# Kernel tuning notes

Measured on AMD Instinct MI355X. Metric: run time of the kernel, lower is better.

## Reference

```python
import jax, jax.numpy as jnp
import numpy as np

N_NODES = 50000
N_EDGES = 800000
D_IN = 128
D_OUT = 128


def setup_inputs() -> dict:
    key = jax.random.key(0)
    k1, k2, k3, k4, k5 = jax.random.split(key, 5)
    gain = float(np.sqrt(2.0))  # calculate_gain('relu')
    # xavier_uniform bound: gain * sqrt(6/(fan_in+fan_out))
    bound = gain * float(np.sqrt(6.0 / (D_IN + D_OUT)))
    feat = jax.random.normal(k1, (N_NODES, D_IN), dtype=jnp.float32)
    weight = jax.random.uniform(k2, (D_IN, D_OUT), minval=-bound, maxval=bound, dtype=jnp.float32)
    loop_weight = jax.random.uniform(k3, (D_IN, D_OUT), minval=-bound, maxval=bound, dtype=jnp.float32)
    h_bias = jnp.zeros((D_OUT,), dtype=jnp.float32)
    src = jax.random.randint(k4, (N_EDGES,), 0, N_NODES, dtype=jnp.int32)
    dst = jax.random.randint(k5, (N_EDGES,), 0, N_NODES, dtype=jnp.int32)
    return {"feat": feat, "weight": weight, "h_bias": h_bias,
            "loop_weight": loop_weight, "src": src, "dst": dst}


def reference(feat, weight, h_bias, loop_weight, src, dst):
    # message: m_e = feat[src_e] @ W ; aggregate: h_v = sum_{e: dst_e=v} m_e
    # (equivalently transform-then-gather, which avoids the [E, D] matmul)
    transformed = feat @ weight                    # [N, D_out]
    msgs = transformed[src]                        # [E, D_out] gather
    h = jax.ops.segment_sum(msgs, dst, num_segments=feat.shape[0])  # [N, D_out]
    h = h + h_bias                                 # bias
    h = h + feat @ loop_weight                     # self-loop
    # activation=None, dropout=0 -> identity
    return h
```

## Files before the change

### kernel.cpp

```cpp
#include <hip/hip_runtime.h>

#define D 128
#define CAP 64
#define FCHUNK 4096
#define LROW 264

typedef __attribute__((ext_vector_type(8))) short bf16x8;
typedef __attribute__((ext_vector_type(4))) float f32x4;

__device__ inline unsigned short f2bf_rne(float x) {
    unsigned u = __float_as_uint(x);
    return (unsigned short)((u + 0x7FFFu + ((u >> 16) & 1u)) >> 16);
}
__device__ inline float bf_lo(unsigned u) { return __uint_as_float(u << 16); }
__device__ inline float bf_hi(unsigned u) { return __uint_as_float(u & 0xFFFF0000u); }

__global__ __launch_bounds__(256) void prep_kernel(
    const float* __restrict__ W, const float* __restrict__ LW,
    unsigned short* __restrict__ Bt, int* __restrict__ cursor, int ncur)
{
    int tid = blockIdx.x * 256 + threadIdx.x;
    if (tid < 2 * D * D) {
        int n = tid >> 7;
        int k = tid & 127;
        float v = (n < D) ? W[(size_t)k * D + n] : LW[(size_t)k * D + (n - D)];
        Bt[(size_t)n * D + k] = f2bf_rne(v);
    }
    int j = tid - 2 * D * D;
    if (j >= 0 && j < ncur) cursor[j] = 0;
}

__global__ __launch_bounds__(256) void fill_kernel(
    const int* __restrict__ src, const int* __restrict__ dst,
    int* __restrict__ cursor, unsigned short* __restrict__ ebuf,
    int E, int cstride)
{
    const int chunk = blockIdx.x >> 3;
    const int cls   = blockIdx.x & 7;
    const int base  = chunk * FCHUNK;

    for (int i = threadIdx.x; i < FCHUNK; i += 256) {
        const int e = base + i;
        if (e >= E) break;
        const int d = dst[e];
        const int s = src[e];
        if ((d & 7) == cls) {
            int pos = atomicAdd(&cursor[(cls * cstride) + (d >> 3)], 1);
            if (pos < CAP) ebuf[(size_t)d * CAP + pos] = (unsigned short)s;
        }
    }
}

__global__ __launch_bounds__(256) void mfma_transform(
    const float* __restrict__ feat, const unsigned short* __restrict__ Bt,
    unsigned short* __restrict__ T2, int N)
{
    __shared__ unsigned short tile[4 * 16 * LROW];
    const int wave = threadIdx.x >> 6;
    const int lane = threadIdx.x & 63;
    const int wrow0 = blockIdx.x * 64 + wave * 16;
    const int m    = lane & 15;
    const int kg   = lane >> 4;

    int arow_idx = wrow0 + m;
    if (arow_idx >= N) arow_idx = N - 1;
    const float* arow = feat + (size_t)arow_idx * D;

    bf16x8 a[4];
#pragma unroll
    for (int ks = 0; ks < 4; ++ks) {
        const float4 f0 = *(const float4*)(arow + ks * 32 + kg * 8);
        const float4 f1 = *(const float4*)(arow + ks * 32 + kg * 8 + 4);
        bf16x8 v;
        v[0] = (short)f2bf_rne(f0.x); v[1] = (short)f2bf_rne(f0.y);
        v[2] = (short)f2bf_rne(f0.z); v[3] = (short)f2bf_rne(f0.w);
        v[4] = (short)f2bf_rne(f1.x); v[5] = (short)f2bf_rne(f1.y);
        v[6] = (short)f2bf_rne(f1.z); v[7] = (short)f2bf_rne(f1.w);
        a[ks] = v;
    }

    f32x4 acc[16];
#pragma unroll
    for (int t = 0; t < 16; ++t) acc[t] = (f32x4){0.f, 0.f, 0.f, 0.f};

#pragma unroll
    for (int t = 0; t < 16; ++t) {
        const unsigned short* brow = Bt + (size_t)(t * 16 + m) * D;
        bf16x8 b0 = *(const bf16x8*)(brow + 0 * 32 + kg * 8);
        bf16x8 b1 = *(const bf16x8*)(brow + 1 * 32 + kg * 8);
        bf16x8 b2 = *(const bf16x8*)(brow + 2 * 32 + kg * 8);
        bf16x8 b3 = *(const bf16x8*)(brow + 3 * 32 + kg * 8);
        acc[t] = __builtin_amdgcn_mfma_f32_16x16x32_bf16(a[0], b0, acc[t], 0, 0, 0);
        acc[t] = __builtin_amdgcn_mfma_f32_16x16x32_bf16(a[1], b1, acc[t], 0, 0, 0);
        acc[t] = __builtin_amdgcn_mfma_f32_16x16x32_bf16(a[2], b2, acc[t], 0, 0, 0);
        acc[t] = __builtin_amdgcn_mfma_f32_16x16x32_bf16(a[3], b3, acc[t], 0, 0, 0);
    }

    unsigned short* wtile = tile + wave * 16 * LROW;
#pragma unroll
    for (int t = 0; t < 16; ++t) {
#pragma unroll
        for (int r = 0; r < 4; ++r)
            wtile[(kg * 4 + r) * LROW + t * 16 + m] = f2bf_rne(acc[t][r]);
    }
    __syncthreads();

#pragma unroll
    for (int i = 0; i < 8; ++i) {
        const int f   = i * 64 + lane;
        const int row = f >> 5;
        const int cs  = f & 31;
        if (wrow0 + row < N) {
            const uint4 v = *(const uint4*)(wtile + row * LROW + cs * 8);
            *(uint4*)(T2 + (size_t)(wrow0 + row) * 256 + cs * 8) = v;
        }
    }
}

__global__ __launch_bounds__(256) void gather_kernel(
    const unsigned short* __restrict__ ebuf, const int* __restrict__ cursor,
    const unsigned short* __restrict__ T2, const float* __restrict__ bias,
    float* __restrict__ out, int N, int cstride)
{
    const int node = (blockIdx.x * 256 + threadIdx.x) >> 6;
    const int lane = threadIdx.x & 63;
    if (node >= N) return;

    const int h = lane >> 5;
    const int q = lane & 31;

    int deg = cursor[((node & 7) * cstride) + (node >> 3)];
    if (deg > CAP) deg = CAP;

    const unsigned* region = (const unsigned*)(ebuf + (size_t)node * CAP);
    const unsigned short* Tq = T2 + q * 4;

    float a0 = 0.f, a1 = 0.f, a2 = 0.f, a3 = 0.f;

    for (int j = 0; j < deg; j += 16) {
        uint2 u[8];
#pragma unroll
        for (int k = 0; k < 8; ++k) {
            const unsigned w = region[(j >> 1) + k];
            const unsigned s = h ? (w >> 16) : (w & 0xFFFFu);
            u[k] = *(const uint2*)(Tq + (size_t)s * 256);
        }
#pragma unroll
        for (int k = 0; k < 8; ++k) {
            const bool live = (j + 2 * k + h) < deg;
            a0 += live ? bf_lo(u[k].x) : 0.f;
            a1 += live ? bf_hi(u[k].x) : 0.f;
            a2 += live ? bf_lo(u[k].y) : 0.f;
            a3 += live ? bf_hi(u[k].y) : 0.f;
        }
    }

    a0 += __shfl_xor(a0, 32, 64);
    a1 += __shfl_xor(a1, 32, 64);
    a2 += __shfl_xor(a2, 32, 64);
    a3 += __shfl_xor(a3, 32, 64);

    if (h == 0) {
        const uint2 sv = *(const uint2*)(T2 + (size_t)node * 256 + 128 + q * 4);
        const float4 b = *(const float4*)(bias + q * 4);
        float4 o;
        o.x = b.x + bf_lo(sv.x) + a0;
        o.y = b.y + bf_hi(sv.x) + a1;
        o.z = b.z + bf_lo(sv.y) + a2;
        o.w = b.w + bf_hi(sv.y) + a3;
        *(float4*)(out + (size_t)node * D + q * 4) = o;
    }
}

extern "C" void kernel_launch(void* const* d_in, const int* in_sizes, int n_in,
                              void* d_out, int out_size, void* d_ws, size_t ws_size,
                              hipStream_t stream) {
    const float* feat = (const float*)d_in[0];
    const float* W    = (const float*)d_in[1];
    const float* bias = (const float*)d_in[2];
    const float* LW   = (const float*)d_in[3];
    const int*   src  = (const int*)d_in[4];
    const int*   dst  = (const int*)d_in[5];
    float* out = (float*)d_out;

    const int N = in_sizes[0] / D;
    const int E = in_sizes[4];
    const int cstride = (N + 7) >> 3;
    const int ncur = 8 * cstride;

    unsigned short* T2   = (unsigned short*)d_ws;
    unsigned short* Bt   = T2 + (size_t)N * 256;
    unsigned short* ebuf = Bt + 2 * D * D;
    int* cursor = (int*)(ebuf + (size_t)N * CAP);

    {
        const int work = 2 * D * D + ncur;
        prep_kernel<<<dim3((work + 255) / 256), 256, 0, stream>>>(W, LW, Bt, cursor, ncur);
    }

    {
        const int nchunks = (E + FCHUNK - 1) / FCHUNK;
        fill_kernel<<<dim3(nchunks * 8), 256, 0, stream>>>(src, dst, cursor, ebuf, E, cstride);
    }

    mfma_transform<<<dim3((N + 63) / 64), 256, 0, stream>>>(feat, Bt, T2, N);

    gather_kernel<<<dim3((N + 3) / 4), 256, 0, stream>>>(ebuf, cursor, T2, bias, out, N, cstride);
}
```

Before: 189.9 us.

## Merge edge bucketing and MFMA transform into one launch; remap gather nodes by class

```diff
diff --git a/kernel.cpp b/kernel.cpp
--- a/kernel.cpp
+++ b/kernel.cpp
@@ -30,35 +30,38 @@
     if (j >= 0 && j < ncur) cursor[j] = 0;
 }
 
-__global__ __launch_bounds__(256) void fill_kernel(
+__global__ __launch_bounds__(256) void fill_mfma_kernel(
     const int* __restrict__ src, const int* __restrict__ dst,
     int* __restrict__ cursor, unsigned short* __restrict__ ebuf,
-    int E, int cstride)
-{
-    const int chunk = blockIdx.x >> 3;
-    const int cls   = blockIdx.x & 7;
-    const int base  = chunk * FCHUNK;
-
-    for (int i = threadIdx.x; i < FCHUNK; i += 256) {
-        const int e = base + i;
-        if (e >= E) break;
-        const int d = dst[e];
-        const int s = src[e];
-        if ((d & 7) == cls) {
-            int pos = atomicAdd(&cursor[(cls * cstride) + (d >> 3)], 1);
-            if (pos < CAP) ebuf[(size_t)d * CAP + pos] = (unsigned short)s;
-        }
-    }
-}
-
-__global__ __launch_bounds__(256) void mfma_transform(
+    int E, int cstride, int nmfma,
     const float* __restrict__ feat, const unsigned short* __restrict__ Bt,
     unsigned short* __restrict__ T2, int N)
 {
     __shared__ unsigned short tile[4 * 16 * LROW];
+    const int b = blockIdx.x;
+
+    if (b >= nmfma) {
+        const int fidx  = b - nmfma;
+        const int cls   = b & 7;
+        const int chunk = fidx >> 3;
+        const int base  = chunk * FCHUNK;
+
+        for (int i = threadIdx.x; i < FCHUNK; i += 256) {
+            const int e = base + i;
+            if (e >= E) break;
+            const int d = dst[e];
+            if ((d & 7) == cls) {
+                const int s = src[e];
+                const int pos = atomicAdd(&cursor[(cls * cstride) + (d >> 3)], 1);
+                if (pos < CAP) ebuf[(size_t)d * CAP + pos] = (unsigned short)s;
+            }
+        }
+        return;
+    }
+
     const int wave = threadIdx.x >> 6;
     const int lane = threadIdx.x & 63;
-    const int wrow0 = blockIdx.x * 64 + wave * 16;
+    const int wrow0 = b * 64 + wave * 16;
     const int m    = lane & 15;
     const int kg   = lane >> 4;
 
@@ -122,14 +125,16 @@
     const unsigned short* __restrict__ T2, const float* __restrict__ bias,
     float* __restrict__ out, int N, int cstride)
 {
-    const int node = (blockIdx.x * 256 + threadIdx.x) >> 6;
+    const int cls  = blockIdx.x & 7;
+    const int w    = threadIdx.x >> 6;
+    const int node = (((int)(blockIdx.x >> 3) * 4 + w) * 8) + cls;
     const int lane = threadIdx.x & 63;
     if (node >= N) return;
 
     const int h = lane >> 5;
     const int q = lane & 31;
 
-    int deg = cursor[((node & 7) * cstride) + (node >> 3)];
+    int deg = cursor[(cls * cstride) + (node >> 3)];
     if (deg > CAP) deg = CAP;
 
     const unsigned* region = (const unsigned*)(ebuf + (size_t)node * CAP);
@@ -141,8 +146,9 @@
         uint2 u[8];
 #pragma unroll
         for (int k = 0; k < 8; ++k) {
-            const unsigned w = region[(j >> 1) + k];
-            const unsigned s = h ? (w >> 16) : (w & 0xFFFFu);
+            const unsigned w32 = region[(j >> 1) + k];
+            unsigned s = h ? (w32 >> 16) : (w32 & 0xFFFFu);
+            if (j + 2 * k + h >= deg) s = 0;
             u[k] = *(const uint2*)(Tq + (size_t)s * 256);
         }
 #pragma unroll
@@ -200,10 +206,15 @@
 
     {
         const int nchunks = (E + FCHUNK - 1) / FCHUNK;
-        fill_kernel<<<dim3(nchunks * 8), 256, 0, stream>>>(src, dst, cursor, ebuf, E, cstride);
-    }
-
-    mfma_transform<<<dim3((N + 63) / 64), 256, 0, stream>>>(feat, Bt, T2, N);
-
-    gather_kernel<<<dim3((N + 3) / 4), 256, 0, stream>>>(ebuf, cursor, T2, bias, out, N, cstride);
-}
+        const int nfill   = nchunks * 8;
+        const int nmfma   = (N + 63) / 64;
+        fill_mfma_kernel<<<dim3(nmfma + nfill), 256, 0, stream>>>(
+            src, dst, cursor, ebuf, E, cstride, nmfma, feat, Bt, T2, N);
+    }
+
+    {
+        const int bpc = (cstride + 3) / 4;
+        gather_kernel<<<dim3(8 * bpc), 256, 0, stream>>>(
+            ebuf, cursor, T2, bias, out, N, cstride);
+    }
+}
```

New measurement: 189.2 us. About the same (-0.3%).
